# Optimization experiments

Measured on AMD Instinct MI355X. Metric: run time of the kernel, lower is better.

Reference implementation:

```python
import jax, jax.numpy as jnp
import numpy as np
from jax import lax

ORDER = 2  # diffusion order per support, as in __init__(order=2)


def setup_inputs() -> dict:
    key = jax.random.key(0)
    k1, k2, k3 = jax.random.split(key, 3)
    N, C, V, L = 64, 32, 512, 13
    S, Kt, C_out = 3, 3, 32
    C_cat = (ORDER * S + 1) * C  # 224
    x = jax.random.normal(k1, (N, C, V, L), dtype=jnp.float32)
    support = jax.random.uniform(k2, (S, V, V), dtype=jnp.float32)
    # Conv2d(c_in=224, c_out=32, kernel=(1,Kt)) weights, PyTorch OIHW layout
    W = jax.random.normal(k3, (C_out, C_cat, 1, Kt), dtype=jnp.float32) * 0.02
    b = jnp.zeros((C_out,), dtype=jnp.float32)
    return {"x": x, "support": support, "W": W, "b": b}


def _nconv(x, A):
    # torch: A = A.T; einsum('ncvl,vw->ncwl', x, A.T)
    # => out[n,c,w,l] = sum_v A[w,v] * x[n,c,v,l]
    return jnp.einsum('ncvl,wv->ncwl', x, A)


def reference(x, support, W, b):
    out = [x]
    for s in range(support.shape[0]):  # small fixed support_len=3
        A = support[s]
        x1 = _nconv(x, A)
        out.append(x1)
        for _ in range(2, ORDER + 1):
            x1 = _nconv(x1, A)
            out.append(x1)
    h = jnp.concatenate(out, axis=1)  # [N, (order*S+1)*C, V, L]
    # Conv2d kernel (1, Kt), no padding, stride 1 -> temporal conv
    y = lax.conv_general_dilated(
        h, W, window_strides=(1, 1), padding='VALID',
        dimension_numbers=('NCHW', 'OIHW', 'NCHW'))
    y = y + b[None, :, None, None]
    # dropout is identity in eval mode
    return y
```

## Files before the change

kernel.cpp:

```cpp
#include <hip/hip_runtime.h>

typedef __attribute__((ext_vector_type(4))) float f32x4;
typedef __attribute__((ext_vector_type(8))) __bf16 bf16x8;
typedef __attribute__((ext_vector_type(4))) __bf16 bf16x4;
typedef __attribute__((ext_vector_type(4))) int i32x4;

#define SXE (26624 * 512)

__global__ __launch_bounds__(256)
void prep_x(const float* __restrict__ x, __bf16* __restrict__ Xv2) {
  const int vt = blockIdx.x, n = blockIdx.y, tid = threadIdx.x;
  __shared__ float Xs[32 * 209];
  const float* src = x + ((size_t)n * 32) * 6656 + vt * 16 * 13;
  for (int i = tid; i < 32 * 208; i += 256) {
    const int c = i / 208, r = i - c * 208;
    Xs[c * 209 + r] = src[(size_t)c * 6656 + r];
  }
  __syncthreads();
  for (int j = tid; j < 416; j += 256) {
    const int c = j & 31, l = j >> 5;
    bf16x8 o8[2];
    #pragma unroll
    for (int v = 0; v < 16; ++v) o8[v >> 3][v & 7] = (__bf16)Xs[c * 209 + v * 13 + l];
    __bf16* d = Xv2 + (((size_t)n * 13 + l) * 32 + c) * 512 + vt * 16;
    *(bf16x8*)d = o8[0];
    *(bf16x8*)(d + 8) = o8[1];
  }
}

__global__ __launch_bounds__(256)
void cast_A(const float* __restrict__ A, __bf16* __restrict__ Ab) {
  const int i = blockIdx.x * 256 + threadIdx.x;
  const float4 f = ((const float4*)A)[i];
  bf16x4 o;
  o[0] = (__bf16)f.x; o[1] = (__bf16)f.y; o[2] = (__bf16)f.z; o[3] = (__bf16)f.w;
  ((bf16x4*)Ab)[i] = o;
}

__global__ __launch_bounds__(256)
void gemm_bf16(const __bf16* __restrict__ Ab, const __bf16* __restrict__ SRC,
               __bf16* __restrict__ DSTB, size_t srcStride, size_t dstStride, int cpx) {
  const int tid = threadIdx.x;
  const int lane = tid & 63, wave = tid >> 6, q = lane >> 4;

  const int bid = blockIdx.x;
  const int lg = (bid & 7) * cpx + (bid >> 3);
  const int bx = lg / 12, r12 = lg % 12, s = r12 >> 2, by = r12 & 3;

  const __bf16* Amat = Ab + (size_t)s * 512 * 512;
  const __bf16* B = SRC + (size_t)s * srcStride;
  __bf16* D = DSTB + (size_t)s * dstStride;

  const int W0 = by * 128, B0 = bx * 128;
  const int wm = wave >> 1, wn = wave & 1;

  __shared__ __bf16 As[128 * 64];
  __shared__ __bf16 Bs[128 * 64];

  f32x4 acc[4][4];
  #pragma unroll
  for (int m = 0; m < 4; ++m)
    #pragma unroll
    for (int n = 0; n < 4; ++n) acc[m][n] = {0.f, 0.f, 0.f, 0.f};

  const int srow = lane >> 3, spos = lane & 7;

  for (int kt = 0; kt < 8; ++kt) {
    const int k0 = kt * 64;
    #pragma unroll
    for (int i = 0; i < 4; ++i) {
      const int slot = i * 4 + wave;
      const int r = slot * 8 + srow;
      const int gc = spos ^ (r & 7);
      const __bf16* ga = Amat + (size_t)(W0 + r) * 512 + k0 + gc * 8;
      const __bf16* gb = B    + (size_t)(B0 + r) * 512 + k0 + gc * 8;
      char* la = (char*)As + slot * 1024 + lane * 16;
      char* lb = (char*)Bs + slot * 1024 + lane * 16;
      __builtin_amdgcn_global_load_lds((const __attribute__((address_space(1))) unsigned int*)ga,
                                       (__attribute__((address_space(3))) unsigned int*)la, 16, 0, 0);
      __builtin_amdgcn_global_load_lds((const __attribute__((address_space(1))) unsigned int*)gb,
                                       (__attribute__((address_space(3))) unsigned int*)lb, 16, 0, 0);
    }
    __syncthreads();
    #pragma unroll
    for (int ks = 0; ks < 2; ++ks) {
      bf16x8 af[4], df[4];
      const int ch = ks * 4 + q;
      #pragma unroll
      for (int m = 0; m < 4; ++m) {
        const int r = wm * 64 + m * 16 + (lane & 15);
        af[m] = *(const bf16x8*)((const char*)As + r * 128 + ((ch ^ (r & 7)) << 4));
      }
      #pragma unroll
      for (int n = 0; n < 4; ++n) {
        const int r = wn * 64 + n * 16 + (lane & 15);
        df[n] = *(const bf16x8*)((const char*)Bs + r * 128 + ((ch ^ (r & 7)) << 4));
      }
      #pragma unroll
      for (int m = 0; m < 4; ++m)
        #pragma unroll
        for (int n = 0; n < 4; ++n)
          acc[m][n] = __builtin_amdgcn_mfma_f32_16x16x32_bf16(af[m], df[n], acc[m][n], 0, 0, 0);
    }
    __syncthreads();
  }

  #pragma unroll
  for (int m = 0; m < 4; ++m) {
    const int w = W0 + wm * 64 + m * 16 + q * 4;
    #pragma unroll
    for (int n = 0; n < 4; ++n) {
      const int b = B0 + wn * 64 + n * 16 + (lane & 15);
      bf16x4 o4;
      o4[0] = (__bf16)acc[m][n][0]; o4[1] = (__bf16)acc[m][n][1];
      o4[2] = (__bf16)acc[m][n][2]; o4[3] = (__bf16)acc[m][n][3];
      *(bf16x4*)(D + (size_t)b * 512 + w) = o4;
    }
  }
}

__global__ __launch_bounds__(256)
void conv_kernel(const __bf16* __restrict__ Xv2, const __bf16* __restrict__ Y1,
                 const __bf16* __restrict__ Y2, const float* __restrict__ W,
                 const float* __restrict__ bias, float* __restrict__ y) {
  const int vt = blockIdx.x;
  const int n  = blockIdx.y;
  const int tid = threadIdx.x;
  const int lane = tid & 63, wave = tid >> 6, q = lane >> 4, r16 = lane & 15;

  __shared__ char sm[59392];
  char* Ws = sm + 53248;

  const __bf16* gsrc[7] = {Xv2, Y1, Y2, Y1 + (size_t)SXE, Y2 + (size_t)SXE,
                           Y1 + 2 * (size_t)SXE, Y2 + 2 * (size_t)SXE};

  f32x4 acc[11][2];
  #pragma unroll
  for (int t = 0; t < 11; ++t) { acc[t][0] = {0,0,0,0}; acc[t][1] = {0,0,0,0}; }

  for (int g = 0; g < 7; ++g) {
    __syncthreads();
    const __bf16* src = gsrc[g] + ((size_t)n * 416) * 512 + vt * 64;
    #pragma unroll
    for (int it = 0; it < 13; ++it) {
      const int idx = it * 256 + tid;
      const int l = idx >> 8, rem = idx & 255, c = rem >> 3, h = rem & 7;
      i32x4 val = *(const i32x4*)(src + ((size_t)(l * 32 + c) << 9) + h * 8);
      *(i32x4*)(sm + l * 4096 + c * 128 + h * 16) = val;
    }
    for (int idx = tid; idx < 768; idx += 256) {
      const int f = idx >> 7, rem2 = idx & 127, lw = rem2 >> 1, half = rem2 & 1;
      const int kt = f >> 1, of = f & 1;
      const int o = of * 16 + (lw & 15);
      const int cc = g * 32 + (lw >> 4) * 8 + half * 4;
      bf16x4 w4;
      #pragma unroll
      for (int j = 0; j < 4; ++j)
        w4[j] = (__bf16)W[((size_t)o * 224 + cc + j) * 3 + kt];
      *(bf16x4*)(Ws + idx * 8) = w4;
    }
    __syncthreads();

    bf16x8 a8[13];
    const int gbase = q * 8 * 128 + (wave * 16 + r16) * 2;
    #pragma unroll
    for (int l = 0; l < 13; ++l) {
      bf16x8 a;
      #pragma unroll
      for (int j = 0; j < 8; ++j)
        a[j] = *(const __bf16*)(sm + l * 4096 + gbase + j * 128);
      a8[l] = a;
    }
    bf16x8 wf[6];
    #pragma unroll
    for (int f = 0; f < 6; ++f)
      wf[f] = *(const bf16x8*)(Ws + (f * 64 + lane) * 16);

    #pragma unroll
    for (int kt = 0; kt < 3; ++kt)
      #pragma unroll
      for (int of = 0; of < 2; ++of)
        #pragma unroll
        for (int t = 0; t < 11; ++t)
          acc[t][of] = __builtin_amdgcn_mfma_f32_16x16x32_bf16(a8[t + kt], wf[kt * 2 + of], acc[t][of], 0, 0, 0);
  }

  float* Ds = (float*)sm;
  const int o16 = lane & 15;
  for (int p = 0; p < 2; ++p) {
    __syncthreads();
    #pragma unroll
    for (int t = 0; t < 11; ++t) {
      const int vbase = wave * 16 + q * 4;
      #pragma unroll
      for (int rg = 0; rg < 4; ++rg)
        Ds[o16 * 708 + (vbase + rg) * 11 + t] = acc[t][p][rg];
    }
    __syncthreads();
    for (int i = 0; i < 11; ++i) {
      const int cg = tid + i * 256;
      const int oo = cg / 176, ch = cg - oo * 176;
      f32x4 v4 = *(const f32x4*)(Ds + oo * 708 + ch * 4);
      const float bo = bias[p * 16 + oo];
      v4[0] += bo; v4[1] += bo; v4[2] += bo; v4[3] += bo;
      float* yp = y + (((size_t)n * 32 + p * 16 + oo) * 512 + vt * 64) * 11 + ch * 4;
      *(f32x4*)yp = v4;
    }
  }
}

extern "C" void kernel_launch(void* const* d_in, const int* in_sizes, int n_in,
                              void* d_out, int out_size, void* d_ws, size_t ws_size,
                              hipStream_t stream) {
  (void)in_sizes; (void)n_in; (void)out_size; (void)ws_size;
  const float* x = (const float*)d_in[0];
  const float* A = (const float*)d_in[1];
  const float* W = (const float*)d_in[2];
  const float* b = (const float*)d_in[3];
  float* y = (float*)d_out;

  char* ws = (char*)d_ws;
  const size_t SXB = (size_t)SXE * 2;
  __bf16* Xv2 = (__bf16*)ws;
  __bf16* Y1  = (__bf16*)(ws + SXB);
  __bf16* Y2  = (__bf16*)(ws + 4 * SXB);
  __bf16* Ab  = (__bf16*)(ws + 7 * SXB);

  cast_A<<<dim3(768), 256, 0, stream>>>(A, Ab);
  prep_x<<<dim3(32, 64), 256, 0, stream>>>(x, Xv2);
  gemm_bf16<<<dim3(2496), 256, 0, stream>>>(Ab, Xv2, Y1, 0, (size_t)SXE, 312);
  gemm_bf16<<<dim3(2496), 256, 0, stream>>>(Ab, Y1, Y2, (size_t)SXE, (size_t)SXE, 312);
  conv_kernel<<<dim3(8, 64), 256, 0, stream>>>(Xv2, Y1, Y2, W, b, y);
}
```

Before: 232.1 us.

## Enlarge GEMM tiles to 256x256 with double-buffered LDS and 512 threads

```diff
diff --git a/kernel.cpp b/kernel.cpp
--- a/kernel.cpp
+++ b/kernel.cpp
@@ -37,80 +37,90 @@
   ((bf16x4*)Ab)[i] = o;
 }
 
-__global__ __launch_bounds__(256)
+__global__ __launch_bounds__(512, 2)
 void gemm_bf16(const __bf16* __restrict__ Ab, const __bf16* __restrict__ SRC,
                __bf16* __restrict__ DSTB, size_t srcStride, size_t dstStride, int cpx) {
+  extern __shared__ char gsm[];
   const int tid = threadIdx.x;
-  const int lane = tid & 63, wave = tid >> 6, q = lane >> 4;
+  const int lane = tid & 63, wid = tid >> 6, q = lane >> 4, r16 = lane & 15;
 
   const int bid = blockIdx.x;
   const int lg = (bid & 7) * cpx + (bid >> 3);
-  const int bx = lg / 12, r12 = lg % 12, s = r12 >> 2, by = r12 & 3;
+  const int bx = lg / 6, r6 = lg % 6, s = r6 >> 1, by = r6 & 1;
 
   const __bf16* Amat = Ab + (size_t)s * 512 * 512;
   const __bf16* B = SRC + (size_t)s * srcStride;
   __bf16* D = DSTB + (size_t)s * dstStride;
 
-  const int W0 = by * 128, B0 = bx * 128;
-  const int wm = wave >> 1, wn = wave & 1;
-
-  __shared__ __bf16 As[128 * 64];
-  __shared__ __bf16 Bs[128 * 64];
-
-  f32x4 acc[4][4];
+  const int W0 = by * 256, B0 = bx * 256;
+  const int wm = wid >> 2, wn = wid & 3;
+  const int srow = lane >> 3, spos = lane & 7;
+
+  f32x4 acc[8][4];
   #pragma unroll
-  for (int m = 0; m < 4; ++m)
+  for (int m = 0; m < 8; ++m)
     #pragma unroll
     for (int n = 0; n < 4; ++n) acc[m][n] = {0.f, 0.f, 0.f, 0.f};
 
-  const int srow = lane >> 3, spos = lane & 7;
-
-  for (int kt = 0; kt < 8; ++kt) {
+  auto STAGE = [&](int bufsel, int kt) {
     const int k0 = kt * 64;
+    char* As = gsm + bufsel * 65536;
+    char* Bs = As + 32768;
     #pragma unroll
     for (int i = 0; i < 4; ++i) {
-      const int slot = i * 4 + wave;
+      const int slot = i * 8 + wid;
       const int r = slot * 8 + srow;
       const int gc = spos ^ (r & 7);
       const __bf16* ga = Amat + (size_t)(W0 + r) * 512 + k0 + gc * 8;
       const __bf16* gb = B    + (size_t)(B0 + r) * 512 + k0 + gc * 8;
-      char* la = (char*)As + slot * 1024 + lane * 16;
-      char* lb = (char*)Bs + slot * 1024 + lane * 16;
       __builtin_amdgcn_global_load_lds((const __attribute__((address_space(1))) unsigned int*)ga,
-                                       (__attribute__((address_space(3))) unsigned int*)la, 16, 0, 0);
+                                       (__attribute__((address_space(3))) unsigned int*)(As + slot * 1024 + lane * 16),
+                                       16, 0, 0);
       __builtin_amdgcn_global_load_lds((const __attribute__((address_space(1))) unsigned int*)gb,
-                                       (__attribute__((address_space(3))) unsigned int*)lb, 16, 0, 0);
-    }
-    __syncthreads();
+                                       (__attribute__((address_space(3))) unsigned int*)(Bs + slot * 1024 + lane * 16),
+                                       16, 0, 0);
+    }
+  };
+
+  STAGE(0, 0);
+  __syncthreads();
+
+  for (int t = 0; t < 8; ++t) {
+    const int cur = t & 1;
+    if (t < 7) STAGE(cur ^ 1, t + 1);
+    const char* As = gsm + cur * 65536;
+    const char* Bs = As + 32768;
     #pragma unroll
     for (int ks = 0; ks < 2; ++ks) {
-      bf16x8 af[4], df[4];
       const int ch = ks * 4 + q;
-      #pragma unroll
-      for (int m = 0; m < 4; ++m) {
-        const int r = wm * 64 + m * 16 + (lane & 15);
-        af[m] = *(const bf16x8*)((const char*)As + r * 128 + ((ch ^ (r & 7)) << 4));
+      bf16x8 af[4], df[8];
+      #pragma unroll
+      for (int n = 0; n < 4; ++n) {
+        const int r = wn * 64 + n * 16 + r16;
+        af[n] = *(const bf16x8*)(As + r * 128 + ((ch ^ (r & 7)) << 4));
       }
       #pragma unroll
-      for (int n = 0; n < 4; ++n) {
-        const int r = wn * 64 + n * 16 + (lane & 15);
-        df[n] = *(const bf16x8*)((const char*)Bs + r * 128 + ((ch ^ (r & 7)) << 4));
+      for (int m = 0; m < 8; ++m) {
+        const int r = wm * 128 + m * 16 + r16;
+        df[m] = *(const bf16x8*)(Bs + r * 128 + ((ch ^ (r & 7)) << 4));
       }
-      #pragma unroll
-      for (int m = 0; m < 4; ++m)
+      __builtin_amdgcn_s_setprio(1);
+      #pragma unroll
+      for (int m = 0; m < 8; ++m)
         #pragma unroll
         for (int n = 0; n < 4; ++n)
-          acc[m][n] = __builtin_amdgcn_mfma_f32_16x16x32_bf16(af[m], df[n], acc[m][n], 0, 0, 0);
+          acc[m][n] = __builtin_amdgcn_mfma_f32_16x16x32_bf16(af[n], df[m], acc[m][n], 0, 0, 0);
+      __builtin_amdgcn_s_setprio(0);
     }
     __syncthreads();
   }
 
   #pragma unroll
-  for (int m = 0; m < 4; ++m) {
-    const int w = W0 + wm * 64 + m * 16 + q * 4;
+  for (int m = 0; m < 8; ++m) {
+    const int b = B0 + wm * 128 + m * 16 + r16;
     #pragma unroll
     for (int n = 0; n < 4; ++n) {
-      const int b = B0 + wn * 64 + n * 16 + (lane & 15);
+      const int w = W0 + wn * 64 + n * 16 + q * 4;
       bf16x4 o4;
       o4[0] = (__bf16)acc[m][n][0]; o4[1] = (__bf16)acc[m][n][1];
       o4[2] = (__bf16)acc[m][n][2]; o4[3] = (__bf16)acc[m][n][3];
@@ -228,7 +238,7 @@
 
   cast_A<<<dim3(768), 256, 0, stream>>>(A, Ab);
   prep_x<<<dim3(32, 64), 256, 0, stream>>>(x, Xv2);
-  gemm_bf16<<<dim3(2496), 256, 0, stream>>>(Ab, Xv2, Y1, 0, (size_t)SXE, 312);
-  gemm_bf16<<<dim3(2496), 256, 0, stream>>>(Ab, Y1, Y2, (size_t)SXE, (size_t)SXE, 312);
+  gemm_bf16<<<dim3(624), 512, 131072, stream>>>(Ab, Xv2, Y1, 0, (size_t)SXE, 78);
+  gemm_bf16<<<dim3(624), 512, 131072, stream>>>(Ab, Y1, Y2, (size_t)SXE, (size_t)SXE, 78);
   conv_kernel<<<dim3(8, 64), 256, 0, stream>>>(Xv2, Y1, Y2, W, b, y);
 }
```

Measured after the change: 231.0 us. Within noise of the previous version (-0.5%).
